# Performance work log

Hardware: AMD Instinct MI355X
Metric: run time of the kernel (lower is better)

## Reference

```python
import jax, jax.numpy as jnp
import numpy as np

OUTDIM = 10
STRIDES = (2, 2, 1)
PADS = (2, 2, 1)  # int((k-1)/2) for k=5,5,3
LEAK = 0.2


def _conv(x, w, b, s, p):
    y = jax.lax.conv_general_dilated(x, w, (s, s), [(p, p), (p, p)],
                                     dimension_numbers=('NCHW', 'OIHW', 'NCHW'))
    return y + b[None, :, None, None]


def _grid(outdim):
    off = (jnp.arange(outdim, dtype=jnp.float32) - (outdim - 1) / 2.0) / outdim
    gx = jnp.broadcast_to(off[None, :], (outdim, outdim))  # varies along j (x)
    gy = jnp.broadcast_to(off[:, None], (outdim, outdim))  # varies along i (y)
    return jnp.stack([gx, gy], axis=-1)  # [od, od, 2]


def _bilinear(img, x, y):
    # img: [C,H,W]; x,y: [N] float. Faithful to original (x clamped by H, y by W).
    H, W = img.shape[-2], img.shape[-1]
    x0 = jnp.floor(x).astype(jnp.int32); x1 = x0 + 1
    y0 = jnp.floor(y).astype(jnp.int32); y1 = y0 + 1
    x0 = jnp.clip(x0, 0, H - 1); x1 = jnp.clip(x1, 0, H - 1)
    y0 = jnp.clip(y0, 0, W - 1); y1 = jnp.clip(y1, 0, W - 1)
    Ia = img[:, y0, x0]; Ib = img[:, y1, x0]; Ic = img[:, y0, x1]; Id = img[:, y1, x1]
    x0f = x0.astype(x.dtype); x1f = x1.astype(x.dtype)
    y0f = y0.astype(y.dtype); y1f = y1.astype(y.dtype)
    step = jnp.clip((x1f - x0f) * (y1f - y0f), 0.001, 2.0)
    inv = 1.0 / step
    wa = (x1f - x) * (y1f - y) * inv
    wb = (x1f - x) * (y - y0f) * inv
    wc = (x - x0f) * (y1f - y) * inv
    wd = (x - x0f) * (y - y0f) * inv
    return Ia * wa + Ib * wb + Ic * wc + Id * wd  # [C, N]


def _roi_one(feat, roi, gg):
    # feat: [C,H,W]; roi: [R,7]
    W1, W2 = roi[:, 2:3], roi[:, 3:4]
    H1, H2 = roi[:, 4:5], roi[:, 5:6]
    psi = roi[:, 6:7]
    WH = jnp.concatenate([W1 + W2, H1 + H2], axis=-1)          # [R,2]
    offset = jnp.concatenate([(W1 - W2) / 2, (H1 - H2) / 2], axis=-1)
    s, c = jnp.sin(psi), jnp.cos(psi)                          # [R,1]
    rotM = jnp.stack([jnp.concatenate([c, -s], -1),
                      jnp.concatenate([s, c], -1)], axis=-2)   # [R,2,2]
    ggi = gg[None] * WH[:, None, None, :] - offset[:, None, None, :]  # [R,od,od,2]
    ggi = jnp.einsum('rijk,rkl->rijl', ggi, rotM) + roi[:, None, None, 0:2]
    xs = ggi[..., 0].reshape(-1)
    ys = ggi[..., 1].reshape(-1)
    samp = _bilinear(feat, xs, ys)                             # [C, R*od*od]
    R, C = roi.shape[0], feat.shape[0]
    # faithful to original .view(R, C, od, od) applied to the [C, N] buffer
    return samp.reshape(R, C, OUTDIM, OUTDIM)


def setup_inputs() -> dict:
    key = jax.random.key(0)
    ks = jax.random.split(key, 12)
    B, R = 32, 32
    x = jax.random.normal(ks[0], (B, 3, 224, 224), dtype=jnp.float32)
    u = jax.random.uniform(ks[1], (B, R, 7), dtype=jnp.float32)
    lo = jnp.array([5., 5., 1., 1., 1., 1., -np.pi], dtype=jnp.float32)
    hi = jnp.array([51., 51., 8., 8., 8., 8., np.pi], dtype=jnp.float32)
    ROI = lo + u * (hi - lo)  # coords in 56x56 feature-map frame
    w1 = jax.random.normal(ks[2], (32, 3, 5, 5), dtype=jnp.float32) * 0.05
    b1 = jnp.zeros((32,), dtype=jnp.float32)
    w2 = jax.random.normal(ks[3], (64, 32, 5, 5), dtype=jnp.float32) * 0.05
    b2 = jnp.zeros((64,), dtype=jnp.float32)
    w3 = jax.random.normal(ks[4], (128, 64, 3, 3), dtype=jnp.float32) * 0.05
    b3 = jnp.zeros((128,), dtype=jnp.float32)
    fc_w = jax.random.normal(ks[5], (256, OUTDIM * OUTDIM * 128), dtype=jnp.float32) * 0.01
    fc_b = jnp.zeros((256,), dtype=jnp.float32)
    return {'x': x, 'ROI': ROI, 'w1': w1, 'b1': b1, 'w2': w2, 'b2': b2,
            'w3': w3, 'b3': b3, 'fc_w': fc_w, 'fc_b': fc_b}


def reference(x, ROI, w1, b1, w2, b2, w3, b3, fc_w, fc_b):
    for (w, b, s, p) in ((w1, b1, STRIDES[0], PADS[0]),
                         (w2, b2, STRIDES[1], PADS[1]),
                         (w3, b3, STRIDES[2], PADS[2])):
        x = jax.nn.leaky_relu(_conv(x, w, b, s, p), LEAK)
    gg = _grid(OUTDIM)
    roi_feat = jax.vmap(lambda f, r: _roi_one(f, r, gg))(x, ROI)  # [B,R,C,od,od]
    B, R = roi_feat.shape[0], roi_feat.shape[1]
    flat = roi_feat.reshape(B, R, -1)
    return flat @ fc_w.T + fc_b  # [B, R, 256]
```

## Files before the change

kernel.cpp:

```cpp
#include <hip/hip_runtime.h>
#include <hip/hip_bf16.h>

#define LEAK 0.2f

__device__ __forceinline__ float lrelu(float a) { return a > 0.0f ? a : LEAK * a; }

typedef __attribute__((ext_vector_type(8))) short short8;
typedef __attribute__((ext_vector_type(4))) float f32x4;

__device__ __forceinline__ unsigned short bf16_hi_bits(float x) {
    unsigned u = __builtin_bit_cast(unsigned, x);
    unsigned r = u + 0x7fffu + ((u >> 16) & 1u);
    return (unsigned short)(r >> 16);
}
__device__ __forceinline__ float bf16_to_f32(unsigned short h) {
    unsigned u = ((unsigned)h) << 16;
    return __builtin_bit_cast(float, u);
}
__device__ __forceinline__ unsigned pack_bf16pair(float x) {
    unsigned short h = bf16_hi_bits(x);
    float lo = x - bf16_to_f32(h);
    return (unsigned)h | ((unsigned)bf16_hi_bits(lo) << 16);
}

__device__ __forceinline__ unsigned pack_lo16(unsigned o, unsigned e) {
    return __builtin_amdgcn_perm(o, e, 0x05040100u);
}
__device__ __forceinline__ unsigned pack_hi16(unsigned o, unsigned e) {
    return __builtin_amdgcn_perm(o, e, 0x07060302u);
}

template<int CI, int ST, int KH, int KW, int KIN, int KP,
         int PIH, int PIW, int LP, int OW, int PPI,
         int CO, int NT, int MR, int NR, int OSH, int OSW, int OR0, int OC0,
         int MINW, int NTHR, int BK>
__global__ __launch_bounds__(NTHR, MINW) void conv_gemm_k(
    const float* __restrict__ in,
    const float* __restrict__ wT,
    const float* __restrict__ bias,
    float* __restrict__ out)
{
    constexpr int KT  = KP / BK;
    constexpr int TXW = NT / 4;
    constexpr int TXN = NT / NR;
    constexpr int BT  = BK * NT / 4;
    constexpr int AT  = BK * CO / 4;
    constexpr int BI  = (BT + NTHR - 1) / NTHR;
    constexpr int AI  = (AT + NTHR - 1) / NTHR;
    constexpr int ASZ = BK * CO;
    constexpr int BSZ = BK * NT;

    __shared__ float sm[2 * ASZ + 2 * BSZ];

    const int tid = threadIdx.x;
    const int bx  = blockIdx.x;
    const int tx  = tid % TXN;
    const int ty  = tid / TXN;

    int bofs[BI], bkl[BI], bcol[BI];
#pragma unroll
    for (int q = 0; q < BI; ++q) {
        int task = tid + q * NTHR;
        if ((BT % NTHR == 0) || task < BT) {
            int kl  = task / TXW;
            int pxq = task % TXW;
            int px0 = bx * NT + pxq * 4;
            int img = px0 / PPI;
            int n   = px0 % PPI;
            int oh  = n / OW, ow = n % OW;
            bofs[q] = ((img * CI) * PIH + oh * ST) * PIW + ow * ST + LP;
            bkl[q]  = kl;
            bcol[q] = (NR == 8) ? (((pxq & 1) * (TXW / 2) + (pxq >> 1)) * 4)
                                : (pxq * 4);
        }
    }

    float  br[BI][4];
    float4 ar[AI];

    auto gather = [&](int it) {
        int k0 = it * BK;
#pragma unroll
        for (int q = 0; q < BI; ++q) {
            int task = tid + q * NTHR;
            if ((BT % NTHR == 0) || task < BT) {
                int k = k0 + bkl[q];
                if (KP > KIN) k = min(k, KIN - 1);
                int ci  = k / (KH * KW);
                int rem = k - ci * (KH * KW);
                int kh  = rem / KW;
                int kw  = rem - kh * KW;
                const float* __restrict__ s = in + bofs[q] + (ci * PIH + kh) * PIW + kw;
                br[q][0] = s[0]; br[q][1] = s[ST]; br[q][2] = s[2 * ST]; br[q][3] = s[3 * ST];
            }
        }
#pragma unroll
        for (int p = 0; p < AI; ++p) {
            int task = tid + p * NTHR;
            if ((AT % NTHR == 0) || task < AT)
                ar[p] = *(const float4*)&wT[(size_t)k0 * CO + task * 4];
        }
    };

    float acc[MR][NR];
#pragma unroll
    for (int j = 0; j < MR; ++j) {
        float bv = bias[ty * MR + j];
#pragma unroll
        for (int i = 0; i < NR; ++i) acc[j][i] = bv;
    }

    gather(0);
    for (int it = 0; it < KT; ++it) {
        const int p = it & 1;
        float* __restrict__ Asb = sm + p * ASZ;
        float* __restrict__ Bsb = sm + 2 * ASZ + p * BSZ;
#pragma unroll
        for (int pa = 0; pa < AI; ++pa) {
            int task = tid + pa * NTHR;
            if ((AT % NTHR == 0) || task < AT)
                *(float4*)&Asb[task * 4] = ar[pa];
        }
#pragma unroll
        for (int q = 0; q < BI; ++q) {
            int task = tid + q * NTHR;
            if ((BT % NTHR == 0) || task < BT)
                *(float4*)&Bsb[bkl[q] * NT + bcol[q]] =
                    make_float4(br[q][0], br[q][1], br[q][2], br[q][3]);
        }
        __syncthreads();
        if (it + 1 < KT) gather(it + 1);
#pragma unroll
        for (int k = 0; k < BK; ++k) {
            float b[NR], a[MR];
            if (NR == 8) {
                *(float4*)&b[0] = *(const float4*)&Bsb[k * NT + tx * 4];
                *(float4*)&b[4] = *(const float4*)&Bsb[k * NT + NT / 2 + tx * 4];
            } else {
#pragma unroll
                for (int i = 0; i < NR / 4; ++i)
                    *(float4*)&b[4 * i] = *(const float4*)&Bsb[k * NT + tx * NR + 4 * i];
            }
#pragma unroll
            for (int j = 0; j < MR / 4; ++j)
                *(float4*)&a[4 * j] = *(const float4*)&Asb[k * CO + ty * MR + 4 * j];
#pragma unroll
            for (int j = 0; j < MR; ++j)
#pragma unroll
                for (int i = 0; i < NR; ++i)
                    acc[j][i] += a[j] * b[i];
        }
    }

    {
        int pxs = bx * NT + tx * NR;
        int img = pxs / PPI;
        int n   = pxs % PPI;
        int oh  = n / OW, ow = n % OW;
#pragma unroll
        for (int j = 0; j < MR; ++j) {
            int co = ty * MR + j;
            size_t off = (((size_t)img * CO + co) * OSH + (oh + OR0)) * OSW + (ow + OC0);
#pragma unroll
            for (int q = 0; q < NR / 4; ++q) {
                float4 v = make_float4(lrelu(acc[j][4 * q + 0]), lrelu(acc[j][4 * q + 1]),
                                       lrelu(acc[j][4 * q + 2]), lrelu(acc[j][4 * q + 3]));
                *(float4*)&out[off + 4 * q] = v;
            }
        }
    }
}

template<int CO, int KIN, int KP>
__global__ __launch_bounds__(256) void wtr_k(const float* __restrict__ w,
                                             float* __restrict__ wT) {
    int i = blockIdx.x * 256 + threadIdx.x;
    if (i >= KP * CO) return;
    int k = i / CO, co = i % CO;
    wT[i] = (k < KIN) ? w[(size_t)co * KIN + k] : 0.0f;
}

template<int CO, int KIN, int KP>
__global__ __launch_bounds__(256) void wtr_pack_k(const float* __restrict__ w,
                                                  unsigned* __restrict__ wTp) {
    int i = blockIdx.x * 256 + threadIdx.x;
    if (i >= KP * CO) return;
    int k = i / CO, co = i % CO;
    float x = (k < KIN) ? w[(size_t)co * KIN + k] : 0.0f;
    wTp[i] = pack_bf16pair(x);
}

__global__ __launch_bounds__(256) void split_pack_k(const float* __restrict__ src,
                                                    unsigned* __restrict__ dst, int n) {
    for (int i = blockIdx.x * 256 + threadIdx.x; i < n; i += gridDim.x * 256) {
        dst[i] = pack_bf16pair(src[i]);
    }
}

template<int CI, int ST, int KH, int KW, int KP,
         int PIH, int PIW, int LP,
         int CO, int OW, int OSH, int OSW, int OR0, int OC0>
__global__ __launch_bounds__(256, 4) void conv_mfma_k(
    const unsigned* __restrict__ src,
    const unsigned* __restrict__ wp,
    const float* __restrict__ bias,
    float* __restrict__ outp)
{
    constexpr int KT = KP / 32;
    __shared__ unsigned ldsu[5120];
    __shared__ int offtab[KP];
    short* const lds = (short*)ldsu;

    const int tid  = threadIdx.x;
    const int lane = tid & 63;
    const int wv   = tid >> 6;
    const int bx   = blockIdx.x;
    const int by   = blockIdx.y;
    const int bz   = blockIdx.z;

    for (int k = tid; k < KP; k += 256) {
        int ci = k / (KH * KW), r = k - ci * (KH * KW);
        int kh = r / KW, kw = r - kh * KW;
        offtab[k] = (ci * PIH + kh) * PIW + kw;
    }
    __syncthreads();

    const int row = lane;
    const int n   = bx * 64 + row;
    const int oh  = n / OW, ow = n % OW;
    const unsigned* __restrict__ bsrc =
        src + ((size_t)(bz * CI) * PIH + oh * ST) * PIW + ow * ST + LP;
    const unsigned* __restrict__ wsrc = wp + (size_t)(wv * 8) * CO + by * 64 + row;

    unsigned Au[8], Bu[8];
    auto gather = [&](int it) {
        const int k0 = it * 32 + wv * 8;
        int4 o0 = *(const int4*)&offtab[k0];
        int4 o1 = *(const int4*)&offtab[k0 + 4];
        const unsigned* __restrict__ wk = wsrc + (size_t)it * 32 * CO;
#pragma unroll
        for (int j = 0; j < 8; ++j) Au[j] = wk[j * CO];
        Bu[0] = bsrc[o0.x]; Bu[1] = bsrc[o0.y]; Bu[2] = bsrc[o0.z]; Bu[3] = bsrc[o0.w];
        Bu[4] = bsrc[o1.x]; Bu[5] = bsrc[o1.y]; Bu[6] = bsrc[o1.z]; Bu[7] = bsrc[o1.w];
    };

    f32x4 acc[2][2] = {};

    const int cw = wv & 1, pw = wv >> 1;
    const int r15 = lane & 15, kg = lane >> 4;

    gather(0);
    for (int it = 0; it < KT; ++it) {
        {
            const int widx = row * 20 + wv * 4;
            uint4 vh, vl;
            vh.x = pack_lo16(Au[1], Au[0]); vl.x = pack_hi16(Au[1], Au[0]);
            vh.y = pack_lo16(Au[3], Au[2]); vl.y = pack_hi16(Au[3], Au[2]);
            vh.z = pack_lo16(Au[5], Au[4]); vl.z = pack_hi16(Au[5], Au[4]);
            vh.w = pack_lo16(Au[7], Au[6]); vl.w = pack_hi16(Au[7], Au[6]);
            *(uint4*)&ldsu[0 * 1280 + widx] = vh;
            *(uint4*)&ldsu[1 * 1280 + widx] = vl;
            vh.x = pack_lo16(Bu[1], Bu[0]); vl.x = pack_hi16(Bu[1], Bu[0]);
            vh.y = pack_lo16(Bu[3], Bu[2]); vl.y = pack_hi16(Bu[3], Bu[2]);
            vh.z = pack_lo16(Bu[5], Bu[4]); vl.z = pack_hi16(Bu[5], Bu[4]);
            vh.w = pack_lo16(Bu[7], Bu[6]); vl.w = pack_hi16(Bu[7], Bu[6]);
            *(uint4*)&ldsu[2 * 1280 + widx] = vh;
            *(uint4*)&ldsu[3 * 1280 + widx] = vl;
        }
        __syncthreads();
        if (it + 1 < KT) gather(it + 1);

        const short* AsH = lds + 0 * 2560;
        const short* AsL = lds + 1 * 2560;
        const short* BsH = lds + 2 * 2560;
        const short* BsL = lds + 3 * 2560;
        short8 aH[2], aL[2], bH[2], bL[2];
#pragma unroll
        for (int tq = 0; tq < 2; ++tq) {
            const int ra = (cw * 32 + tq * 16 + r15) * 40 + kg * 8;
            aH[tq] = *(const short8*)&AsH[ra];
            aL[tq] = *(const short8*)&AsL[ra];
            const int rb = (pw * 32 + tq * 16 + r15) * 40 + kg * 8;
            bH[tq] = *(const short8*)&BsH[rb];
            bL[tq] = *(const short8*)&BsL[rb];
        }
#pragma unroll
        for (int ct = 0; ct < 2; ++ct)
#pragma unroll
            for (int pt = 0; pt < 2; ++pt) {
                acc[ct][pt] = __builtin_amdgcn_mfma_f32_16x16x32_bf16(aH[ct], bH[pt], acc[ct][pt], 0, 0, 0);
                acc[ct][pt] = __builtin_amdgcn_mfma_f32_16x16x32_bf16(aH[ct], bL[pt], acc[ct][pt], 0, 0, 0);
                acc[ct][pt] = __builtin_amdgcn_mfma_f32_16x16x32_bf16(aL[ct], bH[pt], acc[ct][pt], 0, 0, 0);
            }
        __syncthreads();
    }

#pragma unroll
    for (int ct = 0; ct < 2; ++ct)
#pragma unroll
        for (int pt = 0; pt < 2; ++pt)
#pragma unroll
            for (int rg = 0; rg < 4; ++rg) {
                int co = by * 64 + cw * 32 + ct * 16 + kg * 4 + rg;
                int px = bx * 64 + pw * 32 + pt * 16 + r15;
                int poh = px / OW, pow_ = px % OW;
                float v = acc[ct][pt][rg] + bias[co];
                outp[((size_t)(bz * CO + co) * OSH + (poh + OR0)) * OSW + (pow_ + OC0)] = lrelu(v);
            }
}

__global__ __launch_bounds__(256, 4) void fc_mfma_k(
    const unsigned* __restrict__ Sp,
    const unsigned* __restrict__ Wp,
    float* __restrict__ part)
{
    __shared__ unsigned ldsu[7680];
    short* const lds = (short*)ldsu;

    const int tid  = threadIdx.x;
    const int lane = tid & 63;
    const int wv   = tid >> 6;
    const int bn = blockIdx.x, bm = blockIdx.y, ks = blockIdx.z;

    const int ra = tid & 127, ca = tid >> 7;
    const int rb = tid & 63,  cb = tid >> 6;
    const unsigned* __restrict__ aptr = Sp + (size_t)(bm * 128 + ra) * 12800 + ks * 800;
    const unsigned* __restrict__ bptr = Wp + (size_t)(bn * 64 + rb) * 12800 + ks * 800;

    unsigned Au[16], Bu[8];
    auto gather = [&](int it) {
        const int k0 = it * 32;
#pragma unroll
        for (int j = 0; j < 8; ++j) {
            Au[j]     = aptr[k0 + ca * 8 + j];
            Au[8 + j] = aptr[k0 + (ca + 2) * 8 + j];
            Bu[j]     = bptr[k0 + cb * 8 + j];
        }
    };

    f32x4 acc[2][4] = {};
    const int r15 = lane & 15, kg = lane >> 4;

    gather(0);
    for (int it = 0; it < 25; ++it) {
        {
            uint4 vh, vl;
            vh.x = pack_lo16(Au[1], Au[0]); vl.x = pack_hi16(Au[1], Au[0]);
            vh.y = pack_lo16(Au[3], Au[2]); vl.y = pack_hi16(Au[3], Au[2]);
            vh.z = pack_lo16(Au[5], Au[4]); vl.z = pack_hi16(Au[5], Au[4]);
            vh.w = pack_lo16(Au[7], Au[6]); vl.w = pack_hi16(Au[7], Au[6]);
            *(uint4*)&ldsu[ra * 20 + ca * 4]        = vh;
            *(uint4*)&ldsu[2560 + ra * 20 + ca * 4] = vl;
            vh.x = pack_lo16(Au[9],  Au[8]);  vl.x = pack_hi16(Au[9],  Au[8]);
            vh.y = pack_lo16(Au[11], Au[10]); vl.y = pack_hi16(Au[11], Au[10]);
            vh.z = pack_lo16(Au[13], Au[12]); vl.z = pack_hi16(Au[13], Au[12]);
            vh.w = pack_lo16(Au[15], Au[14]); vl.w = pack_hi16(Au[15], Au[14]);
            *(uint4*)&ldsu[ra * 20 + (ca + 2) * 4]        = vh;
            *(uint4*)&ldsu[2560 + ra * 20 + (ca + 2) * 4] = vl;
            vh.x = pack_lo16(Bu[1], Bu[0]); vl.x = pack_hi16(Bu[1], Bu[0]);
            vh.y = pack_lo16(Bu[3], Bu[2]); vl.y = pack_hi16(Bu[3], Bu[2]);
            vh.z = pack_lo16(Bu[5], Bu[4]); vl.z = pack_hi16(Bu[5], Bu[4]);
            vh.w = pack_lo16(Bu[7], Bu[6]); vl.w = pack_hi16(Bu[7], Bu[6]);
            *(uint4*)&ldsu[5120 + rb * 20 + cb * 4] = vh;
            *(uint4*)&ldsu[6400 + rb * 20 + cb * 4] = vl;
        }
        __syncthreads();
        if (it + 1 < 25) gather(it + 1);

        const short* AsH = lds;
        const short* AsL = AsH + 5120;
        const short* BsH = AsH + 10240;
        const short* BsL = AsH + 12800;
        short8 aH[2], aL[2], bH[4], bL[4];
#pragma unroll
        for (int mq = 0; mq < 2; ++mq) {
            const int rr = (wv * 32 + mq * 16 + r15) * 40 + kg * 8;
            aH[mq] = *(const short8*)&AsH[rr];
            aL[mq] = *(const short8*)&AsL[rr];
        }
#pragma unroll
        for (int nq = 0; nq < 4; ++nq) {
            const int rr = (nq * 16 + r15) * 40 + kg * 8;
            bH[nq] = *(const short8*)&BsH[rr];
            bL[nq] = *(const short8*)&BsL[rr];
        }
#pragma unroll
        for (int mq = 0; mq < 2; ++mq)
#pragma unroll
            for (int nq = 0; nq < 4; ++nq) {
                acc[mq][nq] = __builtin_amdgcn_mfma_f32_16x16x32_bf16(aH[mq], bH[nq], acc[mq][nq], 0, 0, 0);
                acc[mq][nq] = __builtin_amdgcn_mfma_f32_16x16x32_bf16(aH[mq], bL[nq], acc[mq][nq], 0, 0, 0);
                acc[mq][nq] = __builtin_amdgcn_mfma_f32_16x16x32_bf16(aL[mq], bH[nq], acc[mq][nq], 0, 0, 0);
            }
        __syncthreads();
    }

    float* __restrict__ po = part + (size_t)ks * 262144;
#pragma unroll
    for (int mq = 0; mq < 2; ++mq)
#pragma unroll
        for (int nq = 0; nq < 4; ++nq)
#pragma unroll
            for (int rg = 0; rg < 4; ++rg) {
                int m = bm * 128 + wv * 32 + mq * 16 + kg * 4 + rg;
                int ncol = bn * 64 + nq * 16 + r15;
                po[(size_t)m * 256 + ncol] = acc[mq][nq][rg];
            }
}

__global__ __launch_bounds__(256) void pad_x_k(const float* __restrict__ x,
                                               float* __restrict__ xp) {
    int blk = blockIdx.x;
    int r4 = blk % 57, ic = blk / 57;
    int wid = threadIdx.x >> 6, lane = threadIdx.x & 63;
    int row = r4 * 4 + wid;
    const float* __restrict__ src = x + (size_t)ic * 224 * 224 + (size_t)(row - 2) * 224;
    float* __restrict__ dst = xp + (size_t)ic * 228 * 228 + (size_t)row * 228;
    bool rok = (row >= 2) && (row < 226);
    for (int c = lane; c < 228; c += 64) {
        float v = 0.0f;
        if (rok && c >= 2 && c < 226) v = src[c - 2];
        dst[c] = v;
    }
}

__global__ __launch_bounds__(256) void zb_c1p_k(float* __restrict__ p) {
    float* base = p + (size_t)blockIdx.x * (116 * 120);
    for (int t = threadIdx.x; t < 928; t += 256) {
        int idx;
        if (t < 480) {
            int r = t / 120, c = t - r * 120;
            int row = (r < 2) ? r : r + 112;
            idx = row * 120 + c;
        } else {
            int s = t - 480;
            int r = s >> 2, c = s & 3;
            int col = (c < 2) ? (c + 2) : (c + 114);
            idx = (r + 2) * 120 + col;
        }
        base[idx] = 0.0f;
    }
}

__global__ __launch_bounds__(64) void zb_c2p_k(float* __restrict__ p) {
    float* base = p + (size_t)blockIdx.x * (58 * 64);
    for (int t = threadIdx.x; t < 240; t += 64) {
        int idx;
        if (t < 128) {
            int r = t >> 6, c = t & 63;
            idx = (r ? 57 : 0) * 64 + c;
        } else {
            int s = t - 128;
            int r = (s >> 1) + 1;
            idx = r * 64 + ((s & 1) ? 60 : 3);
        }
        base[idx] = 0.0f;
    }
}

__global__ __launch_bounds__(256) void roi_k(const float* __restrict__ feat,
                                             const float* __restrict__ roi,
                                             unsigned* __restrict__ S) {
    int b = blockIdx.x >> 5;
    int r = blockIdx.x & 31;
    const float* rr = roi + (size_t)(b * 32 + r) * 7;

    __shared__ int   offA[100], offB[100], offC[100], offD[100];
    __shared__ float wA[100], wB[100], wC[100], wD[100];

    int tid = threadIdx.x;
    if (tid < 100) {
        int i = tid / 10, j = tid % 10;
        float cx = rr[0], cy = rr[1];
        float W1 = rr[2], W2 = rr[3], H1 = rr[4], H2 = rr[5], psi = rr[6];
        float offx = ((float)j - 4.5f) / 10.0f;
        float offy = ((float)i - 4.5f) / 10.0f;
        float gx = offx * (W1 + W2) - (W1 - W2) * 0.5f;
        float gy = offy * (H1 + H2) - (H1 - H2) * 0.5f;
        float sn = sinf(psi), cs = cosf(psi);
        float xs = gx * cs + gy * sn + cx;
        float ys = -gx * sn + gy * cs + cy;

        float x0f = floorf(xs), y0f = floorf(ys);
        int x0 = (int)x0f, x1 = x0 + 1;
        int y0 = (int)y0f, y1 = y0 + 1;
        x0 = min(max(x0, 0), 55); x1 = min(max(x1, 0), 55);
        y0 = min(max(y0, 0), 55); y1 = min(max(y1, 0), 55);
        float fx0 = (float)x0, fx1 = (float)x1;
        float fy0 = (float)y0, fy1 = (float)y1;
        float step = (fx1 - fx0) * (fy1 - fy0);
        step = fminf(fmaxf(step, 0.001f), 2.0f);
        float inv = 1.0f / step;
        wA[tid] = (fx1 - xs) * (fy1 - ys) * inv;
        wB[tid] = (fx1 - xs) * (ys - fy0) * inv;
        wC[tid] = (xs - fx0) * (fy1 - ys) * inv;
        wD[tid] = (xs - fx0) * (ys - fy0) * inv;
        offA[tid] = y0 * 56 + x0;
        offB[tid] = y1 * 56 + x0;
        offC[tid] = y0 * 56 + x1;
        offD[tid] = y1 * 56 + x1;
    }
    __syncthreads();

    const float* __restrict__ fb = feat + (size_t)b * 128 * 3136;
    unsigned* __restrict__ outb = S + ((size_t)b * 128 * 32 + r) * 100;
    int c = tid / 100;
    int p = tid - c * 100;
    for (int t = tid; t < 12800; t += 256) {
        const float* f = fb + c * 3136;
        float v = wA[p] * f[offA[p]] + wB[p] * f[offB[p]] +
                  wC[p] * f[offC[p]] + wD[p] * f[offD[p]];
        outb[(size_t)c * 3200 + p] = pack_bf16pair(v);
        p += 56; c += 2;
        if (p >= 100) { p -= 100; ++c; }
    }
}

__global__ __launch_bounds__(256) void fc2_reduce_k(const float* __restrict__ part,
                                                    const float* __restrict__ bias,
                                                    float* __restrict__ out) {
    int i = blockIdx.x * 256 + threadIdx.x;
    float s = bias[i & 255];
    for (int ks = 0; ks < 16; ++ks) s += part[(size_t)ks * 262144 + i];
    out[i] = s;
}

extern "C" void kernel_launch(void* const* d_in, const int* in_sizes, int n_in,
                              void* d_out, int out_size, void* d_ws, size_t ws_size,
                              hipStream_t stream) {
    const float* x   = (const float*)d_in[0];
    const float* ROI = (const float*)d_in[1];
    const float* w1  = (const float*)d_in[2];
    const float* b1  = (const float*)d_in[3];
    const float* w2  = (const float*)d_in[4];
    const float* b2  = (const float*)d_in[5];
    const float* w3  = (const float*)d_in[6];
    const float* b3  = (const float*)d_in[7];
    const float* fcw = (const float*)d_in[8];
    const float* fcb = (const float*)d_in[9];
    float* out = (float*)d_out;

    char* ws = (char*)d_ws;
    float* c1p  = (float*)(ws);
    float* c2p  = (float*)(ws + 57016320);
    float* xpad = (float*)(ws + 87425024);
    float* wT1  = (float*)(ws + 107386880);
    unsigned* wT2p = (unsigned*)(ws + 107397120);
    unsigned* wT3p = (unsigned*)(ws + 107601920);
    float* c3   = (float*)(ws);
    unsigned* S = (unsigned*)(ws + 57016320);
    unsigned* wfcp = (unsigned*)(ws);
    float* part = (float*)(ws + 16777216);

    wtr_k<32, 75, 80><<<10, 256, 0, stream>>>(w1, wT1);
    wtr_pack_k<64, 800, 800><<<200, 256, 0, stream>>>(w2, wT2p);
    wtr_pack_k<128, 576, 576><<<288, 256, 0, stream>>>(w3, wT3p);
    pad_x_k<<<32 * 3 * 57, 256, 0, stream>>>(x, xpad);
    zb_c1p_k<<<1024, 256, 0, stream>>>(c1p);
    zb_c2p_k<<<2048, 64, 0, stream>>>(c2p);

    conv_gemm_k<3, 2, 5, 5, 75, 80, 228, 228, 0, 112, 12544,
                32, 128, 4, 4, 116, 120, 2, 4, 4, 256, 16>
        <<<3136, 256, 0, stream>>>(xpad, wT1, b1, c1p);

    split_pack_k<<<4096, 256, 0, stream>>>(c1p, (unsigned*)c1p, 14254080);
    conv_mfma_k<32, 2, 5, 5, 800, 116, 120, 2, 64, 56, 58, 64, 1, 4>
        <<<dim3(49, 1, 32), 256, 0, stream>>>((unsigned*)c1p, wT2p, b2, c2p);

    split_pack_k<<<4096, 256, 0, stream>>>(c2p, (unsigned*)c2p, 7602176);
    conv_mfma_k<64, 1, 3, 3, 576, 58, 64, 3, 128, 56, 56, 56, 0, 0>
        <<<dim3(49, 2, 32), 256, 0, stream>>>((unsigned*)c2p, wT3p, b3, c3);

    roi_k<<<1024, 256, 0, stream>>>(c3, ROI, S);
    split_pack_k<<<4096, 256, 0, stream>>>(fcw, wfcp, 3276800);
    fc_mfma_k<<<dim3(4, 8, 16), 256, 0, stream>>>(S, wfcp, part);
    fc2_reduce_k<<<1024, 256, 0, stream>>>(part, fcb, out);
}
```

Baseline: 426.7 us.

## Move conv1 to split-bf16 MFMA and fuse bf16 packing into conv epilogues

Replaces the FP32 SIMT conv1 GEMM with an MFMA kernel that uses split bf16 (hi/lo) operands and three MFMAs per tile. The input padding kernel now writes packed bf16 pairs directly. Conv1 and conv2 also emit packed outputs in their epilogues, which removes two standalone split_pack passes over large activation buffers. The aim is to cut FP32 FMA work and extra memory traffic. The cost is a small loss of precision from dropping the lo×lo term, plus scattered gathers through an offset table.

Result: faster. 371.2 us (-13.0%).

```diff
diff --git a/kernel.cpp b/kernel.cpp
--- a/kernel.cpp
+++ b/kernel.cpp
@@ -28,156 +28,6 @@
 }
 __device__ __forceinline__ unsigned pack_hi16(unsigned o, unsigned e) {
     return __builtin_amdgcn_perm(o, e, 0x07060302u);
-}
-
-template<int CI, int ST, int KH, int KW, int KIN, int KP,
-         int PIH, int PIW, int LP, int OW, int PPI,
-         int CO, int NT, int MR, int NR, int OSH, int OSW, int OR0, int OC0,
-         int MINW, int NTHR, int BK>
-__global__ __launch_bounds__(NTHR, MINW) void conv_gemm_k(
-    const float* __restrict__ in,
-    const float* __restrict__ wT,
-    const float* __restrict__ bias,
-    float* __restrict__ out)
-{
-    constexpr int KT  = KP / BK;
-    constexpr int TXW = NT / 4;
-    constexpr int TXN = NT / NR;
-    constexpr int BT  = BK * NT / 4;
-    constexpr int AT  = BK * CO / 4;
-    constexpr int BI  = (BT + NTHR - 1) / NTHR;
-    constexpr int AI  = (AT + NTHR - 1) / NTHR;
-    constexpr int ASZ = BK * CO;
-    constexpr int BSZ = BK * NT;
-
-    __shared__ float sm[2 * ASZ + 2 * BSZ];
-
-    const int tid = threadIdx.x;
-    const int bx  = blockIdx.x;
-    const int tx  = tid % TXN;
-    const int ty  = tid / TXN;
-
-    int bofs[BI], bkl[BI], bcol[BI];
-#pragma unroll
-    for (int q = 0; q < BI; ++q) {
-        int task = tid + q * NTHR;
-        if ((BT % NTHR == 0) || task < BT) {
-            int kl  = task / TXW;
-            int pxq = task % TXW;
-            int px0 = bx * NT + pxq * 4;
-            int img = px0 / PPI;
-            int n   = px0 % PPI;
-            int oh  = n / OW, ow = n % OW;
-            bofs[q] = ((img * CI) * PIH + oh * ST) * PIW + ow * ST + LP;
-            bkl[q]  = kl;
-            bcol[q] = (NR == 8) ? (((pxq & 1) * (TXW / 2) + (pxq >> 1)) * 4)
-                                : (pxq * 4);
-        }
-    }
-
-    float  br[BI][4];
-    float4 ar[AI];
-
-    auto gather = [&](int it) {
-        int k0 = it * BK;
-#pragma unroll
-        for (int q = 0; q < BI; ++q) {
-            int task = tid + q * NTHR;
-            if ((BT % NTHR == 0) || task < BT) {
-                int k = k0 + bkl[q];
-                if (KP > KIN) k = min(k, KIN - 1);
-                int ci  = k / (KH * KW);
-                int rem = k - ci * (KH * KW);
-                int kh  = rem / KW;
-                int kw  = rem - kh * KW;
-                const float* __restrict__ s = in + bofs[q] + (ci * PIH + kh) * PIW + kw;
-                br[q][0] = s[0]; br[q][1] = s[ST]; br[q][2] = s[2 * ST]; br[q][3] = s[3 * ST];
-            }
-        }
-#pragma unroll
-        for (int p = 0; p < AI; ++p) {
-            int task = tid + p * NTHR;
-            if ((AT % NTHR == 0) || task < AT)
-                ar[p] = *(const float4*)&wT[(size_t)k0 * CO + task * 4];
-        }
-    };
-
-    float acc[MR][NR];
-#pragma unroll
-    for (int j = 0; j < MR; ++j) {
-        float bv = bias[ty * MR + j];
-#pragma unroll
-        for (int i = 0; i < NR; ++i) acc[j][i] = bv;
-    }
-
-    gather(0);
-    for (int it = 0; it < KT; ++it) {
-        const int p = it & 1;
-        float* __restrict__ Asb = sm + p * ASZ;
-        float* __restrict__ Bsb = sm + 2 * ASZ + p * BSZ;
-#pragma unroll
-        for (int pa = 0; pa < AI; ++pa) {
-            int task = tid + pa * NTHR;
-            if ((AT % NTHR == 0) || task < AT)
-                *(float4*)&Asb[task * 4] = ar[pa];
-        }
-#pragma unroll
-        for (int q = 0; q < BI; ++q) {
-            int task = tid + q * NTHR;
-            if ((BT % NTHR == 0) || task < BT)
-                *(float4*)&Bsb[bkl[q] * NT + bcol[q]] =
-                    make_float4(br[q][0], br[q][1], br[q][2], br[q][3]);
-        }
-        __syncthreads();
-        if (it + 1 < KT) gather(it + 1);
-#pragma unroll
-        for (int k = 0; k < BK; ++k) {
-            float b[NR], a[MR];
-            if (NR == 8) {
-                *(float4*)&b[0] = *(const float4*)&Bsb[k * NT + tx * 4];
-                *(float4*)&b[4] = *(const float4*)&Bsb[k * NT + NT / 2 + tx * 4];
-            } else {
-#pragma unroll
-                for (int i = 0; i < NR / 4; ++i)
-                    *(float4*)&b[4 * i] = *(const float4*)&Bsb[k * NT + tx * NR + 4 * i];
-            }
-#pragma unroll
-            for (int j = 0; j < MR / 4; ++j)
-                *(float4*)&a[4 * j] = *(const float4*)&Asb[k * CO + ty * MR + 4 * j];
-#pragma unroll
-            for (int j = 0; j < MR; ++j)
-#pragma unroll
-                for (int i = 0; i < NR; ++i)
-                    acc[j][i] += a[j] * b[i];
-        }
-    }
-
-    {
-        int pxs = bx * NT + tx * NR;
-        int img = pxs / PPI;
-        int n   = pxs % PPI;
-        int oh  = n / OW, ow = n % OW;
-#pragma unroll
-        for (int j = 0; j < MR; ++j) {
-            int co = ty * MR + j;
-            size_t off = (((size_t)img * CO + co) * OSH + (oh + OR0)) * OSW + (ow + OC0);
-#pragma unroll
-            for (int q = 0; q < NR / 4; ++q) {
-                float4 v = make_float4(lrelu(acc[j][4 * q + 0]), lrelu(acc[j][4 * q + 1]),
-                                       lrelu(acc[j][4 * q + 2]), lrelu(acc[j][4 * q + 3]));
-                *(float4*)&out[off + 4 * q] = v;
-            }
-        }
-    }
-}
-
-template<int CO, int KIN, int KP>
-__global__ __launch_bounds__(256) void wtr_k(const float* __restrict__ w,
-                                             float* __restrict__ wT) {
-    int i = blockIdx.x * 256 + threadIdx.x;
-    if (i >= KP * CO) return;
-    int k = i / CO, co = i % CO;
-    wT[i] = (k < KIN) ? w[(size_t)co * KIN + k] : 0.0f;
 }
 
 template<int CO, int KIN, int KP>
@@ -197,14 +47,133 @@
     }
 }
 
+__global__ __launch_bounds__(256, 4) void conv1_mfma_k(
+    const unsigned* __restrict__ src,
+    const unsigned* __restrict__ wp,
+    const float* __restrict__ bias,
+    unsigned* __restrict__ outp)
+{
+    __shared__ unsigned ldsu[6400];
+    __shared__ int offtab[96];
+    short* const lds = (short*)ldsu;
+
+    const int tid  = threadIdx.x;
+    const int lane = tid & 63;
+    const int wv   = tid >> 6;
+    const int bx   = blockIdx.x;
+    const int bz   = blockIdx.y;
+
+    if (tid < 96) {
+        int k = min(tid, 74);
+        int ci = k / 25, r = k - ci * 25;
+        int kh = r / 5, kw = r - kh * 5;
+        offtab[tid] = (ci * 228 + kh) * 228 + kw;
+    }
+    __syncthreads();
+
+    const int brow = tid & 127, half = tid >> 7;
+    const int bn   = bx * 128 + brow;
+    const int boh  = bn / 112, bow = bn % 112;
+    const unsigned* __restrict__ bsrc =
+        src + ((size_t)(bz * 3) * 228 + boh * 2) * 228 + bow * 2;
+    const int arow = tid & 31, ks = (tid >> 5) & 3;
+
+    unsigned Bu[16], Au[8];
+    auto gather = [&](int it) {
+        const int k0 = it * 32;
+#pragma unroll
+        for (int c = 0; c < 2; ++c) {
+            int kb = k0 + (half * 2 + c) * 8;
+            int4 o0 = *(const int4*)&offtab[kb];
+            int4 o1 = *(const int4*)&offtab[kb + 4];
+            Bu[c * 8 + 0] = bsrc[o0.x]; Bu[c * 8 + 1] = bsrc[o0.y];
+            Bu[c * 8 + 2] = bsrc[o0.z]; Bu[c * 8 + 3] = bsrc[o0.w];
+            Bu[c * 8 + 4] = bsrc[o1.x]; Bu[c * 8 + 5] = bsrc[o1.y];
+            Bu[c * 8 + 6] = bsrc[o1.z]; Bu[c * 8 + 7] = bsrc[o1.w];
+        }
+        if (tid < 128) {
+            const unsigned* __restrict__ wk = wp + (size_t)(k0 + ks * 8) * 32 + arow;
+#pragma unroll
+            for (int j = 0; j < 8; ++j) Au[j] = wk[j * 32];
+        }
+    };
+
+    f32x4 acc[2][2] = {};
+    const int r15 = lane & 15, kg = lane >> 4;
+
+    gather(0);
+    for (int it = 0; it < 3; ++it) {
+        {
+            uint4 vh, vl;
+#pragma unroll
+            for (int c = 0; c < 2; ++c) {
+                vh.x = pack_lo16(Bu[c*8+1], Bu[c*8+0]); vl.x = pack_hi16(Bu[c*8+1], Bu[c*8+0]);
+                vh.y = pack_lo16(Bu[c*8+3], Bu[c*8+2]); vl.y = pack_hi16(Bu[c*8+3], Bu[c*8+2]);
+                vh.z = pack_lo16(Bu[c*8+5], Bu[c*8+4]); vl.z = pack_hi16(Bu[c*8+5], Bu[c*8+4]);
+                vh.w = pack_lo16(Bu[c*8+7], Bu[c*8+6]); vl.w = pack_hi16(Bu[c*8+7], Bu[c*8+6]);
+                *(uint4*)&ldsu[1280 + brow * 20 + (half * 2 + c) * 4] = vh;
+                *(uint4*)&ldsu[3840 + brow * 20 + (half * 2 + c) * 4] = vl;
+            }
+            if (tid < 128) {
+                vh.x = pack_lo16(Au[1], Au[0]); vl.x = pack_hi16(Au[1], Au[0]);
+                vh.y = pack_lo16(Au[3], Au[2]); vl.y = pack_hi16(Au[3], Au[2]);
+                vh.z = pack_lo16(Au[5], Au[4]); vl.z = pack_hi16(Au[5], Au[4]);
+                vh.w = pack_lo16(Au[7], Au[6]); vl.w = pack_hi16(Au[7], Au[6]);
+                *(uint4*)&ldsu[arow * 20 + ks * 4]       = vh;
+                *(uint4*)&ldsu[640 + arow * 20 + ks * 4] = vl;
+            }
+        }
+        __syncthreads();
+        if (it + 1 < 3) gather(it + 1);
+
+        const short* AsH = lds;
+        const short* AsL = lds + 1280;
+        const short* BsH = lds + 2560;
+        const short* BsL = lds + 7680;
+        short8 aH[2], aL[2], bH[2], bL[2];
+#pragma unroll
+        for (int tq = 0; tq < 2; ++tq) {
+            const int ra = (tq * 16 + r15) * 40 + kg * 8;
+            aH[tq] = *(const short8*)&AsH[ra];
+            aL[tq] = *(const short8*)&AsL[ra];
+            const int rb = (wv * 32 + tq * 16 + r15) * 40 + kg * 8;
+            bH[tq] = *(const short8*)&BsH[rb];
+            bL[tq] = *(const short8*)&BsL[rb];
+        }
+#pragma unroll
+        for (int ct = 0; ct < 2; ++ct)
+#pragma unroll
+            for (int pt = 0; pt < 2; ++pt) {
+                acc[ct][pt] = __builtin_amdgcn_mfma_f32_16x16x32_bf16(aH[ct], bH[pt], acc[ct][pt], 0, 0, 0);
+                acc[ct][pt] = __builtin_amdgcn_mfma_f32_16x16x32_bf16(aH[ct], bL[pt], acc[ct][pt], 0, 0, 0);
+                acc[ct][pt] = __builtin_amdgcn_mfma_f32_16x16x32_bf16(aL[ct], bH[pt], acc[ct][pt], 0, 0, 0);
+            }
+        __syncthreads();
+    }
+
+#pragma unroll
+    for (int ct = 0; ct < 2; ++ct)
+#pragma unroll
+        for (int pt = 0; pt < 2; ++pt)
+#pragma unroll
+            for (int rg = 0; rg < 4; ++rg) {
+                int co = ct * 16 + kg * 4 + rg;
+                int px = bx * 128 + wv * 32 + pt * 16 + r15;
+                int poh = px / 112, pw_ = px % 112;
+                float v = acc[ct][pt][rg] + bias[co];
+                outp[((size_t)(bz * 32 + co) * 116 + poh + 2) * 120 + pw_ + 4] =
+                    pack_bf16pair(lrelu(v));
+            }
+}
+
 template<int CI, int ST, int KH, int KW, int KP,
          int PIH, int PIW, int LP,
-         int CO, int OW, int OSH, int OSW, int OR0, int OC0>
+         int CO, int OW, int OSH, int OSW, int OR0, int OC0, bool POUT>
 __global__ __launch_bounds__(256, 4) void conv_mfma_k(
     const unsigned* __restrict__ src,
     const unsigned* __restrict__ wp,
     const float* __restrict__ bias,
-    float* __restrict__ outp)
+    void* __restrict__ outv)
 {
     constexpr int KT = KP / 32;
     __shared__ unsigned ldsu[5120];
@@ -304,8 +273,10 @@
                 int co = by * 64 + cw * 32 + ct * 16 + kg * 4 + rg;
                 int px = bx * 64 + pw * 32 + pt * 16 + r15;
                 int poh = px / OW, pow_ = px % OW;
-                float v = acc[ct][pt][rg] + bias[co];
-                outp[((size_t)(bz * CO + co) * OSH + (poh + OR0)) * OSW + (pow_ + OC0)] = lrelu(v);
+                float v = lrelu(acc[ct][pt][rg] + bias[co]);
+                size_t off = ((size_t)(bz * CO + co) * OSH + (poh + OR0)) * OSW + (pow_ + OC0);
+                if (POUT) ((unsigned*)outv)[off] = pack_bf16pair(v);
+                else      ((float*)outv)[off]    = v;
             }
 }
 
@@ -409,18 +380,18 @@
 }
 
 __global__ __launch_bounds__(256) void pad_x_k(const float* __restrict__ x,
-                                               float* __restrict__ xp) {
+                                               unsigned* __restrict__ xp) {
     int blk = blockIdx.x;
     int r4 = blk % 57, ic = blk / 57;
     int wid = threadIdx.x >> 6, lane = threadIdx.x & 63;
     int row = r4 * 4 + wid;
     const float* __restrict__ src = x + (size_t)ic * 224 * 224 + (size_t)(row - 2) * 224;
-    float* __restrict__ dst = xp + (size_t)ic * 228 * 228 + (size_t)row * 228;
+    unsigned* __restrict__ dst = xp + (size_t)ic * 228 * 228 + (size_t)row * 228;
     bool rok = (row >= 2) && (row < 226);
     for (int c = lane; c < 228; c += 64) {
         float v = 0.0f;
         if (rok && c >= 2 && c < 226) v = src[c - 2];
-        dst[c] = v;
+        dst[c] = pack_bf16pair(v);
     }
 }
 
@@ -541,35 +512,31 @@
     float* out = (float*)d_out;
 
     char* ws = (char*)d_ws;
-    float* c1p  = (float*)(ws);
-    float* c2p  = (float*)(ws + 57016320);
-    float* xpad = (float*)(ws + 87425024);
-    float* wT1  = (float*)(ws + 107386880);
-    unsigned* wT2p = (unsigned*)(ws + 107397120);
-    unsigned* wT3p = (unsigned*)(ws + 107601920);
+    unsigned* c1p  = (unsigned*)(ws);
+    unsigned* c2p  = (unsigned*)(ws + 57016320);
+    unsigned* xpad = (unsigned*)(ws + 87425024);
+    unsigned* wT1p = (unsigned*)(ws + 107386880);
+    unsigned* wT2p = (unsigned*)(ws + 107399168);
+    unsigned* wT3p = (unsigned*)(ws + 107603968);
     float* c3   = (float*)(ws);
     unsigned* S = (unsigned*)(ws + 57016320);
     unsigned* wfcp = (unsigned*)(ws);
     float* part = (float*)(ws + 16777216);
 
-    wtr_k<32, 75, 80><<<10, 256, 0, stream>>>(w1, wT1);
+    wtr_pack_k<32, 75, 96><<<12, 256, 0, stream>>>(w1, wT1p);
     wtr_pack_k<64, 800, 800><<<200, 256, 0, stream>>>(w2, wT2p);
     wtr_pack_k<128, 576, 576><<<288, 256, 0, stream>>>(w3, wT3p);
     pad_x_k<<<32 * 3 * 57, 256, 0, stream>>>(x, xpad);
-    zb_c1p_k<<<1024, 256, 0, stream>>>(c1p);
-    zb_c2p_k<<<2048, 64, 0, stream>>>(c2p);
-
-    conv_gemm_k<3, 2, 5, 5, 75, 80, 228, 228, 0, 112, 12544,
-                32, 128, 4, 4, 116, 120, 2, 4, 4, 256, 16>
-        <<<3136, 256, 0, stream>>>(xpad, wT1, b1, c1p);
-
-    split_pack_k<<<4096, 256, 0, stream>>>(c1p, (unsigned*)c1p, 14254080);
-    conv_mfma_k<32, 2, 5, 5, 800, 116, 120, 2, 64, 56, 58, 64, 1, 4>
-        <<<dim3(49, 1, 32), 256, 0, stream>>>((unsigned*)c1p, wT2p, b2, c2p);
-
-    split_pack_k<<<4096, 256, 0, stream>>>(c2p, (unsigned*)c2p, 7602176);
-    conv_mfma_k<64, 1, 3, 3, 576, 58, 64, 3, 128, 56, 56, 56, 0, 0>
-        <<<dim3(49, 2, 32), 256, 0, stream>>>((unsigned*)c2p, wT3p, b3, c3);
+    zb_c1p_k<<<1024, 256, 0, stream>>>((float*)c1p);
+    zb_c2p_k<<<2048, 64, 0, stream>>>((float*)c2p);
+
+    conv1_mfma_k<<<dim3(98, 32), 256, 0, stream>>>(xpad, wT1p, b1, c1p);
+
+    conv_mfma_k<32, 2, 5, 5, 800, 116, 120, 2, 64, 56, 58, 64, 1, 4, true>
+        <<<dim3(49, 1, 32), 256, 0, stream>>>(c1p, wT2p, b2, c2p);
+
+    conv_mfma_k<64, 1, 3, 3, 576, 58, 64, 3, 128, 56, 56, 56, 0, 0, false>
+        <<<dim3(49, 2, 32), 256, 0, stream>>>(c2p, wT3p, b3, c3);
 
     roi_k<<<1024, 256, 0, stream>>>(c3, ROI, S);
     split_pack_k<<<4096, 256, 0, stream>>>(fcw, wfcp, 3276800);
```
